# Kernel tuning notes

Measured on AMD Instinct MI355X. Metric: run time of the kernel, lower is better.

Reference implementation:

```python
import jax, jax.numpy as jnp
import numpy as np

NS, NH, NL, NP, E = 2, 8, 4, 4, 256
HD = E // NH  # 32


def grid_sample_zeros(img, grid):
    """torch.F.grid_sample(mode='bilinear', padding_mode='zeros', align_corners=False).
    img: [B, C, Hs, Ws]; grid: [B, Hg, Wg, 2] with (x, y) in [-1, 1]. Returns [B, C, Hg, Wg]."""
    B, C, Hs, Ws = img.shape
    gx = (grid[..., 0] + 1.0) * (Ws * 0.5) - 0.5  # pixel-space x
    gy = (grid[..., 1] + 1.0) * (Hs * 0.5) - 0.5  # pixel-space y
    x0 = jnp.floor(gx)
    y0 = jnp.floor(gy)
    x1, y1 = x0 + 1.0, y0 + 1.0
    wx1 = gx - x0
    wx0 = 1.0 - wx1
    wy1 = gy - y0
    wy0 = 1.0 - wy1
    imgf = img.reshape(B, C, Hs * Ws)

    def gather(ix, iy):
        valid = (ix >= 0) & (ix < Ws) & (iy >= 0) & (iy < Hs)
        ixc = jnp.clip(ix, 0, Ws - 1).astype(jnp.int32)
        iyc = jnp.clip(iy, 0, Hs - 1).astype(jnp.int32)
        flat = (iyc * Ws + ixc).reshape(B, 1, -1)
        vals = jnp.take_along_axis(imgf, flat, axis=2).reshape(B, C, *ix.shape[1:])
        return vals * valid[:, None].astype(img.dtype)

    return (gather(x0, y0) * (wx0 * wy0)[:, None]
            + gather(x1, y0) * (wx1 * wy0)[:, None]
            + gather(x0, y1) * (wx0 * wy1)[:, None]
            + gather(x1, y1) * (wx1 * wy1)[:, None])


def setup_inputs() -> dict:
    key = jax.random.key(0)
    ks = jax.random.split(key, 10)
    bs, Q = 2048, NL * NP  # num_query forced to num_levels*num_points = 16
    f = jnp.float32
    s = 1.0 / np.sqrt(E)
    return {
        "query": jax.random.normal(ks[0], (bs, Q, E), f),
        "key_hist": jax.random.normal(ks[1], (bs, Q, E), f),
        "value_hist": jax.random.normal(ks[2], (bs, Q, E), f),
        "reference_points": jax.random.uniform(ks[3], (bs, Q, NL, 2), f),
        "spatial_shapes": jnp.full((NL, 2), 2, dtype=jnp.int32),  # each level 2x2, sum HW = 16
        "Wq": jax.random.normal(ks[4], (E, E), f) * s, "bq": jnp.zeros((E,), f),
        "Wk": jax.random.normal(ks[5], (E, E), f) * s, "bk": jnp.zeros((E,), f),
        "Wv": jax.random.normal(ks[6], (E, E), f) * s, "bv": jnp.zeros((E,), f),
        "Woff": jax.random.normal(ks[7], (E, NH * NL * NP * 2), f) * (0.01 * s), "boff": jnp.zeros((NH * NL * NP * 2,), f),
        "Wout": jax.random.normal(ks[8], (E, E), f) * s, "bout": jnp.zeros((E,), f),
    }


def reference(query, key_hist, value_hist, reference_points, spatial_shapes,
              Wq, bq, Wk, bk, Wv, bv, Woff, boff, Wout, bout):
    bs, Q, _ = query.shape
    B = bs * NS
    residual = query

    # torch cat(dim=1)+view interleaves the two sequences per batch: index 2b -> query, 2b+1 -> hist
    queries = jnp.repeat(query, NS, axis=0)                              # [B, Q, E]
    keys = jnp.stack([query, key_hist], axis=1).reshape(B, Q, E)
    values = jnp.stack([query, value_hist], axis=1).reshape(B, Q, E)
    rp = jnp.repeat(reference_points, NS, axis=0)                        # [B, Q, NL, 2] (both copies identical)

    qh = (queries @ Wq + bq).reshape(B, Q, NH, HD)
    kh = (keys @ Wk + bk).reshape(B, Q, NH, HD)
    vh = (values @ Wv + bv).reshape(B, Q, NH, HD)

    attn = jax.nn.softmax(jnp.einsum('bqhd,bkhd->bqhk', qh, kh), axis=-1)
    attn = attn.reshape(B, Q, NH, NL, NP)

    offsets = (queries @ Woff + boff).reshape(B, Q, NH, NL, NP, 2)
    norm = jnp.stack([spatial_shapes[:, 1], spatial_shapes[:, 0]], axis=-1).astype(query.dtype)  # (W, H)
    loc = rp[:, :, None, :, None, :] + offsets / norm[None, None, None, :, None, :]
    grid = 2.0 * loc - 1.0                                               # [B, Q, NH, NL, NP, 2]

    ss = np.asarray(spatial_shapes)                                      # static level shapes
    attw = attn.transpose(0, 2, 1, 3, 4).reshape(B * NH, Q, NL, NP)      # [BH, Q, NL, NP]
    acc = jnp.zeros((B * NH, HD, Q), dtype=query.dtype)
    start = 0
    for l in range(NL):
        H_, W_ = int(ss[l, 0]), int(ss[l, 1])
        hw = H_ * W_
        v_l = vh[:, start:start + hw].transpose(0, 2, 3, 1).reshape(B * NH, HD, H_, W_)
        g_l = grid[:, :, :, l].transpose(0, 2, 1, 3, 4).reshape(B * NH, Q, NP, 2)
        s_l = grid_sample_zeros(v_l, g_l)                                # [BH, HD, Q, NP]
        acc = acc + jnp.sum(s_l * attw[:, None, :, l, :], axis=-1)       # weighted reduce over points
        start += hw

    out = acc.reshape(B, E, Q).transpose(0, 2, 1)                        # [B, Q, E]
    out = out.reshape(bs, NS, Q, E).mean(axis=1)                         # mean over the two sequences
    return out @ Wout + bout + residual                                  # dropout is identity in eval
```

## Files before the change

kernel.cpp:

```cpp
#include <hip/hip_runtime.h>

typedef float  f32x4  __attribute__((ext_vector_type(4)));
typedef __bf16 bf16x8 __attribute__((ext_vector_type(8)));
typedef __bf16 bf16x4 __attribute__((ext_vector_type(4)));

__device__ __forceinline__ bf16x8 cvt8(float4 a, float4 b) {
    bf16x8 r;
    r[0] = (__bf16)a.x; r[1] = (__bf16)a.y; r[2] = (__bf16)a.z; r[3] = (__bf16)a.w;
    r[4] = (__bf16)b.x; r[5] = (__bf16)b.y; r[6] = (__bf16)b.z; r[7] = (__bf16)b.w;
    return r;
}

#define OF_OFF 524288
#define PV_OFF (1u << 20)

__global__ void wprep(const float* __restrict__ Wq, const float* __restrict__ Wk,
                      const float* __restrict__ Wv, const float* __restrict__ Woff,
                      const float* __restrict__ Wout, __bf16* __restrict__ ws) {
    int id = blockIdx.x * 256 + threadIdx.x;
    if (id < 262144) {
        int tile = id >> 9, e = id & 511;
        int lane = e >> 3, j = e & 7;
        int kt = tile & 7, nh = (tile >> 3) & 1, mat = (tile >> 4) & 3, h = tile >> 6;
        int k = kt * 32 + (lane >> 4) * 8 + j;
        int col = h * 32 + nh * 16 + (lane & 15);
        const float* W = (mat == 0) ? Wq : (mat == 1) ? Wk : (mat == 2) ? Wv : Woff;
        ws[id] = (__bf16)W[k * 256 + col];
    } else {
        int i = id - 262144;
        int tile = i >> 9, e = i & 511;
        int lane = e >> 3, j = e & 7;
        int kt = tile & 7, nt = tile >> 3;
        int k = kt * 32 + (lane >> 4) * 8 + j;
        int col = nt * 16 + (lane & 15);
        ws[262144 + i] = (__bf16)Wout[k * 256 + col];
    }
}

__launch_bounds__(512, 4)
__global__ void tsa_one(const float* __restrict__ query, const float* __restrict__ keyh,
                        const float* __restrict__ valh, const float* __restrict__ refpts,
                        unsigned char* __restrict__ wsw,
                        const float* __restrict__ bq, const float* __restrict__ bk,
                        const float* __restrict__ bv, const float* __restrict__ boff,
                        const float* __restrict__ bout, float* __restrict__ out, int b0)
{
    __shared__ __attribute__((aligned(16))) unsigned char uni[32768];
    __shared__ __attribute__((aligned(16))) unsigned char scr_all[24576];
    const int t = threadIdx.x;
    const int lane = t & 63, w = t >> 6, l15 = lane & 15, lhi = lane >> 4;
    const int p = w >> 1;
    const int role = w & 1;
    const long b = (long)b0 + (long)blockIdx.x * 4 + p;
    unsigned char* scrp = scr_all + p * 6144;
    __bf16* pvg = (__bf16*)(wsw + PV_OFF) + ((long)blockIdx.x * 4 + p) * 4096;

    bf16x8 afr[8], avr[8];
    {
        const float* s0 = (role ? keyh : query) + b * 4096 + l15 * 256;
        #pragma unroll
        for (int kt = 0; kt < 8; ++kt) {
            int o = kt * 32 + lhi * 8;
            afr[kt] = cvt8(*(const float4*)(s0 + o), *(const float4*)(s0 + o + 4));
        }
        if (role) {
            const float* s1 = valh + b * 4096 + l15 * 256;
            #pragma unroll
            for (int kt = 0; kt < 8; ++kt) {
                int o = kt * 32 + lhi * 8;
                avr[kt] = cvt8(*(const float4*)(s1 + o), *(const float4*)(s1 + o + 4));
            }
        }
    }
    const f32x4 z = (f32x4){0.f, 0.f, 0.f, 0.f};

    for (int h = 0; h < 8; ++h) {
        #pragma unroll 2
        for (int nh = 0; nh < 2; ++nh) {
            __syncthreads();
            #pragma unroll
            for (int it = 0; it < 4; ++it) {
                int u = t + it * 512;
                int f = u >> 6;
                const void* src = (const void*)(wsw +
                    ((((h * 4 + (f >> 3)) * 2 + nh) * 8 + (f & 7)) << 10) + (u & 63) * 16);
                __builtin_amdgcn_global_load_lds(
                    (const __attribute__((address_space(1))) unsigned int*)src,
                    (__attribute__((address_space(3))) unsigned int*)(uni + u * 16),
                    16, 0, 0);
            }
            __syncthreads();
            f32x4 acc[4];
            #pragma unroll
            for (int i = 0; i < 4; ++i) acc[i] = z;
            #pragma unroll
            for (int kt = 0; kt < 8; ++kt) {
                const unsigned char* bb = uni + kt * 1024 + lane * 16;
                bf16x8 b_k = *(const bf16x8*)(bb + 8192);
                bf16x8 b_v = *(const bf16x8*)(bb + 16384);
                if (!role) {
                    bf16x8 b_q = *(const bf16x8*)(bb);
                    bf16x8 b_o = *(const bf16x8*)(bb + 24576);
                    acc[0] = __builtin_amdgcn_mfma_f32_16x16x32_bf16(afr[kt], b_q, acc[0], 0, 0, 0);
                    acc[1] = __builtin_amdgcn_mfma_f32_16x16x32_bf16(afr[kt], b_k, acc[1], 0, 0, 0);
                    acc[2] = __builtin_amdgcn_mfma_f32_16x16x32_bf16(afr[kt], b_v, acc[2], 0, 0, 0);
                    acc[3] = __builtin_amdgcn_mfma_f32_16x16x32_bf16(afr[kt], b_o, acc[3], 0, 0, 0);
                } else {
                    acc[0] = __builtin_amdgcn_mfma_f32_16x16x32_bf16(afr[kt], b_k, acc[0], 0, 0, 0);
                    acc[1] = __builtin_amdgcn_mfma_f32_16x16x32_bf16(avr[kt], b_v, acc[1], 0, 0, 0);
                }
            }
            {
                int dcol = nh * 16 + l15;
                int gcol = h * 32 + dcol;
                if (!role) {
                    float bqv = bq[gcol], bkv = bk[gcol], bvv = bv[gcol], bov = boff[gcol];
                    #pragma unroll
                    for (int r = 0; r < 4; ++r) {
                        int row = lhi * 4 + r;
                        *(__bf16*)(scrp + row * 64 + dcol * 2)        = (__bf16)(acc[0][r] + bqv);
                        *(__bf16*)(scrp + 1024 + row * 64 + dcol * 2) = (__bf16)(acc[1][r] + bkv);
                        *(__bf16*)(scrp + 3072 + dcol * 64 + row * 2) = (__bf16)(acc[2][r] + bvv);
                        *(__bf16*)(scrp + 5120 + row * 64 + dcol * 2) = (__bf16)(acc[3][r] + bov);
                    }
                } else {
                    float bkv = bk[gcol], bvv = bv[gcol];
                    #pragma unroll
                    for (int r = 0; r < 4; ++r) {
                        int row = lhi * 4 + r;
                        *(__bf16*)(scrp + 2048 + row * 64 + dcol * 2)      = (__bf16)(acc[0][r] + bkv);
                        *(__bf16*)(scrp + 3072 + dcol * 64 + 32 + row * 2) = (__bf16)(acc[1][r] + bvv);
                    }
                }
            }
        }
        __syncthreads();

        bf16x8 qf = *(const bf16x8*)(scrp + l15 * 64 + lhi * 16);
        bf16x8 kf = *(const bf16x8*)(scrp + 1024 + role * 1024 + l15 * 64 + lhi * 16);
        f32x4 S = __builtin_amdgcn_mfma_f32_16x16x32_bf16(kf, qf, z, 0, 0, 0);
        float pr[4];
        {
            float m = fmaxf(fmaxf(S[0], S[1]), fmaxf(S[2], S[3]));
            m = fmaxf(m, __shfl_xor(m, 16)); m = fmaxf(m, __shfl_xor(m, 32));
            float s = 0.f;
            #pragma unroll
            for (int r = 0; r < 4; ++r) { pr[r] = __expf(S[r] - m); s += pr[r]; }
            s += __shfl_xor(s, 16); s += __shfl_xor(s, 32);
            float inv = 1.f / s;
            #pragma unroll
            for (int r = 0; r < 4; ++r) pr[r] *= inv;
        }

        {
            float2 rp = *(const float2*)(refpts + b * 128 + l15 * 8 + lhi * 2);
            bf16x8 off8 = *(const bf16x8*)(scrp + 5120 + l15 * 64 + lhi * 16);
            float w4[4] = {0.f, 0.f, 0.f, 0.f};
            #pragma unroll
            for (int pp = 0; pp < 4; ++pp) {
                float gx = 2.f * rp.x + (float)off8[2 * pp]     - 0.5f;
                float gy = 2.f * rp.y + (float)off8[2 * pp + 1] - 0.5f;
                float tx0 = fmaxf(0.f, 1.f - fabsf(gx));
                float tx1 = fmaxf(0.f, 1.f - fabsf(gx - 1.f));
                float ty0 = fmaxf(0.f, 1.f - fabsf(gy));
                float ty1 = fmaxf(0.f, 1.f - fabsf(gy - 1.f));
                w4[0] += tx0 * ty0 * pr[pp]; w4[1] += tx1 * ty0 * pr[pp];
                w4[2] += tx0 * ty1 * pr[pp]; w4[3] += tx1 * ty1 * pr[pp];
            }
            *(bf16x4*)(scrp + 1024 + role * 1024 + l15 * 64 + lhi * 8) =
                (bf16x4){(__bf16)w4[0], (__bf16)w4[1], (__bf16)w4[2], (__bf16)w4[3]};
        }
        __syncthreads();

        {
            bf16x8 aW = *(const bf16x8*)(scrp + 1024 + (lhi >> 1) * 1024 + l15 * 64 + (lhi & 1) * 16);
            bf16x8 vf = *(const bf16x8*)(scrp + 3072 + (role * 16 + l15) * 64 + lhi * 16);
            f32x4 c = __builtin_amdgcn_mfma_f32_16x16x32_bf16(aW, vf, z, 0, 0, 0);
            #pragma unroll
            for (int r = 0; r < 4; ++r) {
                int qq = lhi * 4 + r;
                *(__bf16*)(scrp + qq * 64 + (role * 16 + l15) * 2) = (__bf16)(0.5f * c[r]);
            }
        }
        __syncthreads();
        if (!role) {
            bf16x8 pvfrag = *(const bf16x8*)(scrp + l15 * 64 + lhi * 16);
            *(bf16x8*)(pvg + h * 512 + lane * 8) = pvfrag;
        }
    }

    __syncthreads();

    {
        bf16x8 pv[8];
        #pragma unroll
        for (int kt = 0; kt < 8; ++kt)
            pv[kt] = *(const bf16x8*)(pvg + kt * 512 + lane * 8);
        for (int qd = 0; qd < 4; ++qd) {
            f32x4 o2[2];
            o2[0] = z; o2[1] = z;
            #pragma unroll
            for (int kt = 0; kt < 8; ++kt) {
                #pragma unroll
                for (int j = 0; j < 2; ++j) {
                    int ntl = role * 2 + j;
                    bf16x8 bfr = *(const bf16x8*)(wsw + OF_OFF + qd * 32768 +
                                                  (ntl * 8 + kt) * 1024 + lane * 16);
                    o2[j] = __builtin_amdgcn_mfma_f32_16x16x32_bf16(pv[kt], bfr, o2[j], 0, 0, 0);
                }
            }
            #pragma unroll
            for (int j = 0; j < 2; ++j) {
                int ntl = role * 2 + j;
                int col = (qd * 4 + ntl) * 16 + l15;
                float bo = bout[col];
                #pragma unroll
                for (int r = 0; r < 4; ++r) {
                    int qq = lhi * 4 + r;
                    long idx = b * 4096 + qq * 256 + col;
                    out[idx] = o2[j][r] + bo + query[idx];
                }
            }
        }
    }
}

extern "C" void kernel_launch(void* const* d_in, const int* in_sizes, int n_in,
                              void* d_out, int out_size, void* d_ws, size_t ws_size,
                              hipStream_t stream) {
    const float* query      = (const float*)d_in[0];
    const float* key_hist   = (const float*)d_in[1];
    const float* value_hist = (const float*)d_in[2];
    const float* refpts     = (const float*)d_in[3];
    const float* Wq   = (const float*)d_in[5];
    const float* bq   = (const float*)d_in[6];
    const float* Wk   = (const float*)d_in[7];
    const float* bk   = (const float*)d_in[8];
    const float* Wv   = (const float*)d_in[9];
    const float* bv   = (const float*)d_in[10];
    const float* Woff = (const float*)d_in[11];
    const float* boff = (const float*)d_in[12];
    const float* Wout = (const float*)d_in[13];
    const float* bout = (const float*)d_in[14];
    float* outp = (float*)d_out;

    const int bs = in_sizes[0] / 4096;
    wprep<<<1280, 256, 0, stream>>>(Wq, Wk, Wv, Woff, Wout, (__bf16*)d_ws);

    long avail = (long)ws_size - (long)PV_OFF;
    int CB = bs;
    if (avail < (long)bs * 8192) {
        CB = (int)(avail / 8192) & ~3;
        if (CB < 4) CB = 4;
    }
    for (int b0 = 0; b0 < bs; b0 += CB) {
        int nb = (bs - b0 < CB ? bs - b0 : CB) / 4;
        tsa_one<<<nb, 512, 0, stream>>>(query, key_hist, value_hist, refpts,
                                        (unsigned char*)d_ws,
                                        bq, bk, bv, boff, bout, outp, b0);
    }
}
```

Before: 94.43 us.

## Triple-buffer weight staging and reassign waves to share B fragments across batch pairs

The weight tiles are now streamed in half-K stages into a three-slot LDS ring. Two stages are issued ahead, and each wait uses vmcnt so that global-to-LDS loads overlap with the MFMA work. Waves are regrouped so that each wave computes one projection (Q+offset, K+V, K-hist, or V-hist) for two batch items at once. This reuses each loaded B fragment across two A operands and splits the work more evenly than the earlier query/key role split. The cost is more LDS (48KB for the weight ring) and more register pressure from holding two A fragment sets per wave, which could reduce occupancy.

```diff
diff --git a/kernel.cpp b/kernel.cpp
--- a/kernel.cpp
+++ b/kernel.cpp
@@ -37,6 +37,23 @@
     }
 }
 
+__device__ __forceinline__ void stage_issue(const unsigned char* wsw, int s,
+                                            unsigned char* buf, int t) {
+    int h = s >> 2, nh = (s >> 1) & 1, half = s & 1;
+    #pragma unroll
+    for (int it = 0; it < 2; ++it) {
+        int u = t + it * 512;
+        int f = u >> 6;
+        int kt = half * 4 + (f & 3);
+        const void* src = (const void*)(wsw +
+            ((((h * 4 + (f >> 2)) * 2 + nh) * 8 + kt) << 10) + (u & 63) * 16);
+        __builtin_amdgcn_global_load_lds(
+            (const __attribute__((address_space(1))) unsigned int*)src,
+            (__attribute__((address_space(3))) unsigned int*)(buf + u * 16),
+            16, 0, 0);
+    }
+}
+
 __launch_bounds__(512, 4)
 __global__ void tsa_one(const float* __restrict__ query, const float* __restrict__ keyh,
                         const float* __restrict__ valh, const float* __restrict__ refpts,
@@ -45,91 +62,106 @@
                         const float* __restrict__ bv, const float* __restrict__ boff,
                         const float* __restrict__ bout, float* __restrict__ out, int b0)
 {
-    __shared__ __attribute__((aligned(16))) unsigned char uni[32768];
+    __shared__ __attribute__((aligned(16))) unsigned char uni[49152];
     __shared__ __attribute__((aligned(16))) unsigned char scr_all[24576];
     const int t = threadIdx.x;
     const int lane = t & 63, w = t >> 6, l15 = lane & 15, lhi = lane >> 4;
-    const int p = w >> 1;
-    const int role = w & 1;
-    const long b = (long)b0 + (long)blockIdx.x * 4 + p;
-    unsigned char* scrp = scr_all + p * 6144;
-    __bf16* pvg = (__bf16*)(wsw + PV_OFF) + ((long)blockIdx.x * 4 + p) * 4096;
-
-    bf16x8 afr[8], avr[8];
+    const int pair = w >> 2, sub = w & 3;
+    const int pa = w >> 1, role = w & 1;
+    const long bA  = (long)b0 + (long)blockIdx.x * 4 + pair * 2;
+    const long bAt = (long)b0 + (long)blockIdx.x * 4 + pa;
+    unsigned char* scrp = scr_all + pa * 6144;
+    unsigned char* sc0 = scr_all + (pair * 2) * 6144;
+    unsigned char* sc1 = sc0 + 6144;
+    __bf16* pvg = (__bf16*)(wsw + PV_OFF) + ((long)blockIdx.x * 4 + pa) * 4096;
+
+    bf16x8 a0[8], a1[8];
     {
-        const float* s0 = (role ? keyh : query) + b * 4096 + l15 * 256;
+        const float* srcp = (sub <= 1 ? query : (sub == 2 ? keyh : valh)) + bA * 4096 + l15 * 256;
         #pragma unroll
         for (int kt = 0; kt < 8; ++kt) {
             int o = kt * 32 + lhi * 8;
-            afr[kt] = cvt8(*(const float4*)(s0 + o), *(const float4*)(s0 + o + 4));
-        }
-        if (role) {
-            const float* s1 = valh + b * 4096 + l15 * 256;
-            #pragma unroll
-            for (int kt = 0; kt < 8; ++kt) {
-                int o = kt * 32 + lhi * 8;
-                avr[kt] = cvt8(*(const float4*)(s1 + o), *(const float4*)(s1 + o + 4));
-            }
-        }
-    }
+            a0[kt] = cvt8(*(const float4*)(srcp + o), *(const float4*)(srcp + o + 4));
+            a1[kt] = cvt8(*(const float4*)(srcp + 4096 + o), *(const float4*)(srcp + 4096 + o + 4));
+        }
+    }
+    const float* bX = (sub == 0) ? bq : (sub == 3) ? bv : bk;
+    const float* bY = (sub == 0) ? boff : bv;
     const f32x4 z = (f32x4){0.f, 0.f, 0.f, 0.f};
+    float2 rp = *(const float2*)(refpts + bAt * 128 + l15 * 8 + lhi * 2);
+
+    stage_issue(wsw, 0, uni, t);
+    stage_issue(wsw, 1, uni + 16384, t);
 
     for (int h = 0; h < 8; ++h) {
-        #pragma unroll 2
-        for (int nh = 0; nh < 2; ++nh) {
-            __syncthreads();
-            #pragma unroll
-            for (int it = 0; it < 4; ++it) {
-                int u = t + it * 512;
-                int f = u >> 6;
-                const void* src = (const void*)(wsw +
-                    ((((h * 4 + (f >> 3)) * 2 + nh) * 8 + (f & 7)) << 10) + (u & 63) * 16);
-                __builtin_amdgcn_global_load_lds(
-                    (const __attribute__((address_space(1))) unsigned int*)src,
-                    (__attribute__((address_space(3))) unsigned int*)(uni + u * 16),
-                    16, 0, 0);
-            }
-            __syncthreads();
-            f32x4 acc[4];
-            #pragma unroll
-            for (int i = 0; i < 4; ++i) acc[i] = z;
-            #pragma unroll
-            for (int kt = 0; kt < 8; ++kt) {
-                const unsigned char* bb = uni + kt * 1024 + lane * 16;
-                bf16x8 b_k = *(const bf16x8*)(bb + 8192);
-                bf16x8 b_v = *(const bf16x8*)(bb + 16384);
-                if (!role) {
-                    bf16x8 b_q = *(const bf16x8*)(bb);
-                    bf16x8 b_o = *(const bf16x8*)(bb + 24576);
-                    acc[0] = __builtin_amdgcn_mfma_f32_16x16x32_bf16(afr[kt], b_q, acc[0], 0, 0, 0);
-                    acc[1] = __builtin_amdgcn_mfma_f32_16x16x32_bf16(afr[kt], b_k, acc[1], 0, 0, 0);
-                    acc[2] = __builtin_amdgcn_mfma_f32_16x16x32_bf16(afr[kt], b_v, acc[2], 0, 0, 0);
-                    acc[3] = __builtin_amdgcn_mfma_f32_16x16x32_bf16(afr[kt], b_o, acc[3], 0, 0, 0);
+        float bx0 = bX[h * 32 + l15], bx1 = bX[h * 32 + 16 + l15];
+        float by0 = 0.f, by1 = 0.f;
+        if (sub <= 1) { by0 = bY[h * 32 + l15]; by1 = bY[h * 32 + 16 + l15]; }
+
+        f32x4 acc0, acc1, acc2, acc3;
+        #pragma unroll
+        for (int c = 0; c < 4; ++c) {
+            const int s = h * 4 + c;
+            __builtin_amdgcn_s_barrier();
+            const int s2 = s + 2;
+            if (s2 < 32) stage_issue(wsw, s2, uni + (s2 % 3) * 16384, t);
+            asm volatile("s_waitcnt vmcnt(4)" ::: "memory");
+            __builtin_amdgcn_s_barrier();
+            __builtin_amdgcn_sched_barrier(0);
+            const unsigned char* buf = uni + (s % 3) * 16384;
+            if ((c & 1) == 0) { acc0 = z; acc1 = z; acc2 = z; acc3 = z; }
+            #pragma unroll
+            for (int ktl = 0; ktl < 4; ++ktl) {
+                const int kt = (c & 1) * 4 + ktl;
+                const unsigned char* bb = buf + ktl * 1024 + lane * 16;
+                if (sub == 0) {
+                    bf16x8 bmq = *(const bf16x8*)(bb);
+                    bf16x8 bmo = *(const bf16x8*)(bb + 12288);
+                    acc0 = __builtin_amdgcn_mfma_f32_16x16x32_bf16(a0[kt], bmq, acc0, 0, 0, 0);
+                    acc1 = __builtin_amdgcn_mfma_f32_16x16x32_bf16(a1[kt], bmq, acc1, 0, 0, 0);
+                    acc2 = __builtin_amdgcn_mfma_f32_16x16x32_bf16(a0[kt], bmo, acc2, 0, 0, 0);
+                    acc3 = __builtin_amdgcn_mfma_f32_16x16x32_bf16(a1[kt], bmo, acc3, 0, 0, 0);
+                } else if (sub == 1) {
+                    bf16x8 bmk = *(const bf16x8*)(bb + 4096);
+                    bf16x8 bmv = *(const bf16x8*)(bb + 8192);
+                    acc0 = __builtin_amdgcn_mfma_f32_16x16x32_bf16(a0[kt], bmk, acc0, 0, 0, 0);
+                    acc1 = __builtin_amdgcn_mfma_f32_16x16x32_bf16(a1[kt], bmk, acc1, 0, 0, 0);
+                    acc2 = __builtin_amdgcn_mfma_f32_16x16x32_bf16(a0[kt], bmv, acc2, 0, 0, 0);
+                    acc3 = __builtin_amdgcn_mfma_f32_16x16x32_bf16(a1[kt], bmv, acc3, 0, 0, 0);
+                } else if (sub == 2) {
+                    bf16x8 bmk = *(const bf16x8*)(bb + 4096);
+                    acc0 = __builtin_amdgcn_mfma_f32_16x16x32_bf16(a0[kt], bmk, acc0, 0, 0, 0);
+                    acc1 = __builtin_amdgcn_mfma_f32_16x16x32_bf16(a1[kt], bmk, acc1, 0, 0, 0);
                 } else {
-                    acc[0] = __builtin_amdgcn_mfma_f32_16x16x32_bf16(afr[kt], b_k, acc[0], 0, 0, 0);
-                    acc[1] = __builtin_amdgcn_mfma_f32_16x16x32_bf16(avr[kt], b_v, acc[1], 0, 0, 0);
-                }
-            }
-            {
-                int dcol = nh * 16 + l15;
-                int gcol = h * 32 + dcol;
-                if (!role) {
-                    float bqv = bq[gcol], bkv = bk[gcol], bvv = bv[gcol], bov = boff[gcol];
-                    #pragma unroll
-                    for (int r = 0; r < 4; ++r) {
-                        int row = lhi * 4 + r;
-                        *(__bf16*)(scrp + row * 64 + dcol * 2)        = (__bf16)(acc[0][r] + bqv);
-                        *(__bf16*)(scrp + 1024 + row * 64 + dcol * 2) = (__bf16)(acc[1][r] + bkv);
-                        *(__bf16*)(scrp + 3072 + dcol * 64 + row * 2) = (__bf16)(acc[2][r] + bvv);
-                        *(__bf16*)(scrp + 5120 + row * 64 + dcol * 2) = (__bf16)(acc[3][r] + bov);
-                    }
-                } else {
-                    float bkv = bk[gcol], bvv = bv[gcol];
-                    #pragma unroll
-                    for (int r = 0; r < 4; ++r) {
-                        int row = lhi * 4 + r;
-                        *(__bf16*)(scrp + 2048 + row * 64 + dcol * 2)      = (__bf16)(acc[0][r] + bkv);
-                        *(__bf16*)(scrp + 3072 + dcol * 64 + 32 + row * 2) = (__bf16)(acc[1][r] + bvv);
+                    bf16x8 bmv = *(const bf16x8*)(bb + 8192);
+                    acc0 = __builtin_amdgcn_mfma_f32_16x16x32_bf16(a0[kt], bmv, acc0, 0, 0, 0);
+                    acc1 = __builtin_amdgcn_mfma_f32_16x16x32_bf16(a1[kt], bmv, acc1, 0, 0, 0);
+                }
+            }
+            if (c & 1) {
+                const int nh = c >> 1;
+                const int dcol = nh * 16 + l15;
+                const float bxv = nh ? bx1 : bx0;
+                const float byv = nh ? by1 : by0;
+                #pragma unroll
+                for (int r = 0; r < 4; ++r) {
+                    const int row = lhi * 4 + r;
+                    if (sub == 0) {
+                        *(__bf16*)(sc0 + row * 64 + dcol * 2) = (__bf16)(acc0[r] + bxv);
+                        *(__bf16*)(sc1 + row * 64 + dcol * 2) = (__bf16)(acc1[r] + bxv);
+                        *(__bf16*)(sc0 + 5120 + row * 64 + dcol * 2) = (__bf16)(acc2[r] + byv);
+                        *(__bf16*)(sc1 + 5120 + row * 64 + dcol * 2) = (__bf16)(acc3[r] + byv);
+                    } else if (sub == 1) {
+                        *(__bf16*)(sc0 + 1024 + row * 64 + dcol * 2) = (__bf16)(acc0[r] + bxv);
+                        *(__bf16*)(sc1 + 1024 + row * 64 + dcol * 2) = (__bf16)(acc1[r] + bxv);
+                        *(__bf16*)(sc0 + 3072 + dcol * 64 + row * 2) = (__bf16)(acc2[r] + byv);
+                        *(__bf16*)(sc1 + 3072 + dcol * 64 + row * 2) = (__bf16)(acc3[r] + byv);
+                    } else if (sub == 2) {
+                        *(__bf16*)(sc0 + 2048 + row * 64 + dcol * 2) = (__bf16)(acc0[r] + bxv);
+                        *(__bf16*)(sc1 + 2048 + row * 64 + dcol * 2) = (__bf16)(acc1[r] + bxv);
+                    } else {
+                        *(__bf16*)(sc0 + 3072 + dcol * 64 + 32 + row * 2) = (__bf16)(acc0[r] + bxv);
+                        *(__bf16*)(sc1 + 3072 + dcol * 64 + 32 + row * 2) = (__bf16)(acc1[r] + bxv);
                     }
                 }
             }
@@ -153,7 +185,6 @@
         }
 
         {
-            float2 rp = *(const float2*)(refpts + b * 128 + l15 * 8 + lhi * 2);
             bf16x8 off8 = *(const bf16x8*)(scrp + 5120 + l15 * 64 + lhi * 16);
             float w4[4] = {0.f, 0.f, 0.f, 0.f};
             #pragma unroll
@@ -175,11 +206,11 @@
         {
             bf16x8 aW = *(const bf16x8*)(scrp + 1024 + (lhi >> 1) * 1024 + l15 * 64 + (lhi & 1) * 16);
             bf16x8 vf = *(const bf16x8*)(scrp + 3072 + (role * 16 + l15) * 64 + lhi * 16);
-            f32x4 c = __builtin_amdgcn_mfma_f32_16x16x32_bf16(aW, vf, z, 0, 0, 0);
+            f32x4 c4 = __builtin_amdgcn_mfma_f32_16x16x32_bf16(aW, vf, z, 0, 0, 0);
             #pragma unroll
             for (int r = 0; r < 4; ++r) {
                 int qq = lhi * 4 + r;
-                *(__bf16*)(scrp + qq * 64 + (role * 16 + l15) * 2) = (__bf16)(0.5f * c[r]);
+                *(__bf16*)(scrp + qq * 64 + (role * 16 + l15) * 2) = (__bf16)(0.5f * c4[r]);
             }
         }
         __syncthreads();
@@ -217,7 +248,7 @@
                 #pragma unroll
                 for (int r = 0; r < 4; ++r) {
                     int qq = lhi * 4 + r;
-                    long idx = b * 4096 + qq * 256 + col;
+                    long idx = bAt * 4096 + qq * 256 + col;
                     out[idx] = o2[j][r] + bo + query[idx];
                 }
             }
```

New measurement: 135.6 us. 1.44x slower.
